# Performance work log

Hardware: AMD Instinct MI355X
Metric: run time of the kernel (lower is better)

Reference implementation:

```python
import jax, jax.numpy as jnp
import numpy as np

B, Q, K, H = 4, 512, 512, 256

def setup_inputs() -> dict:
    key = jax.random.key(0)
    ks = jax.random.split(key, 6)
    scale = 1.0 / np.sqrt(H)
    return {
        "queries": jax.random.normal(ks[0], (B, Q, H), dtype=jnp.float32),
        "keys": jax.random.normal(ks[1], (B, K, H), dtype=jnp.float32),
        "values": jax.random.normal(ks[2], (B, K, H), dtype=jnp.float32),
        "W_q": jax.random.normal(ks[3], (H, H), dtype=jnp.float32) * scale,
        "W_k": jax.random.normal(ks[4], (H, H), dtype=jnp.float32) * scale,
        "w_v": jax.random.normal(ks[5], (H,), dtype=jnp.float32) * scale,
    }

def reference(queries, keys, values, W_q, W_k, w_v):
    # Linear (no bias): x @ W.T, matching torch nn.Linear convention
    q = jnp.einsum('bqh,oh->bqo', queries, W_q)      # [B,Q,H]
    k = jnp.einsum('bkh,oh->bko', keys, W_k)          # [B,K,H]
    # broadcast add -> tanh -> linear reduce to scores [B,Q,K]
    features = jnp.tanh(q[:, :, None, :] + k[:, None, :, :])  # [B,Q,K,H]
    scores = jnp.einsum('bqkh,h->bqk', features, w_v)          # [B,Q,K]
    attn = jax.nn.softmax(scores, axis=-1)                     # [B,Q,K]
    # dropout p=0 (eval) -> identity
    return jnp.einsum('bqk,bkd->bqd', attn, values)            # [B,Q,Dv]
```

## Files before the change

### kernel.cpp

```cpp
#include <hip/hip_runtime.h>
#include <hip/hip_bf16.h>
#include <math.h>


#define B_ 4
#define Q_ 512
#define K_ 512
#define H_ 256
#define QE_ELEMS (B_ * Q_ * H_)
#define KE_ELEMS (B_ * H_ * K_)

static constexpr float CEXP = 2.8853900817779268f;
static constexpr float LOG2E = 1.4426950408889634f;

typedef float v2f __attribute__((ext_vector_type(2)));
typedef float v4f __attribute__((ext_vector_type(4)));

__device__ __forceinline__ v2f pk_fma(v2f a, v2f b, v2f c) {
    v2f d;
    asm("v_pk_fma_f32 %0, %1, %2, %3" : "=v"(d) : "v"(a), "v"(b), "v"(c));
    return d;
}
__device__ __forceinline__ v2f pk_fma_l(v2f a, v2f b, v2f c) {
    v2f d;
    asm("v_pk_fma_f32 %0, %1, %2, %3 op_sel:[0,0,0] op_sel_hi:[0,1,1]"
        : "=v"(d) : "v"(a), "v"(b), "v"(c));
    return d;
}
__device__ __forceinline__ v2f pk_fma_h(v2f a, v2f b, v2f c) {
    v2f d;
    asm("v_pk_fma_f32 %0, %1, %2, %3 op_sel:[1,0,0] op_sel_hi:[1,1,1]"
        : "=v"(d) : "v"(a), "v"(b), "v"(c));
    return d;
}
__device__ __forceinline__ v2f pk_mul(v2f a, v2f b) {
    v2f d;
    asm("v_pk_mul_f32 %0, %1, %2" : "=v"(d) : "v"(a), "v"(b));
    return d;
}
__device__ __forceinline__ v2f pk_mul_h(v2f a, v2f b) {
    v2f d;
    asm("v_pk_mul_f32 %0, %1, %2 op_sel:[1,0] op_sel_hi:[1,1]"
        : "=v"(d) : "v"(a), "v"(b));
    return d;
}

#define PJ_AS(team, buf, dd, row) smem[(((team)*2 + (buf)) * 16 + (dd)) * 68 + (row)]
#define PJ_SS(team, buf, dd, row) smem[8704 + (((team)*2 + (buf)) * 16 + (dd)) * 68 + (row)]

__global__ __launch_bounds__(1024, 4) void proj_exp(
    const float* __restrict__ queries, const float* __restrict__ keys,
    const float* __restrict__ Wq, const float* __restrict__ Wk,
    float* __restrict__ qe, float* __restrict__ ke)
{
    __shared__ __align__(16) float smem[17408];

    const int bid = blockIdx.x;
    const int team = threadIdx.x >> 8;
    const int tid = threadIdx.x & 255;

    const float* A; const float* S; float* C; int ldc;
    if (bid < 128) {
        int mt = bid >> 2, nt = bid & 3;
        A = queries + (mt * 64) * H_;
        S = Wq + (nt * 64) * H_;
        C = qe + (mt * 64) * H_ + nt * 64;
        ldc = H_;
    } else {
        int id = bid - 128;
        int b = id >> 5, mt = (id >> 3) & 3, nt = id & 7;
        A = Wk + (mt * 64) * H_;
        S = keys + ((long)(b * K_ + nt * 64)) * H_;
        C = ke + ((long)(b * H_ + mt * 64)) * K_ + nt * 64;
        ldc = K_;
    }

    const int tx = tid & 15;
    const int ty = tid >> 4;
    const int ldr = tid >> 2;
    const int ldd = (tid & 3) * 4;
    const float* GA = A + ldr * H_ + team * 64 + ldd;
    const float* GS = S + ldr * H_ + team * 64 + ldd;

    float4 av = *(const float4*)GA;
    float4 sv = *(const float4*)GS;
    PJ_AS(team, 0, ldd + 0, ldr) = av.x; PJ_AS(team, 0, ldd + 1, ldr) = av.y;
    PJ_AS(team, 0, ldd + 2, ldr) = av.z; PJ_AS(team, 0, ldd + 3, ldr) = av.w;
    PJ_SS(team, 0, ldd + 0, ldr) = sv.x; PJ_SS(team, 0, ldd + 1, ldr) = sv.y;
    PJ_SS(team, 0, ldd + 2, ldr) = sv.z; PJ_SS(team, 0, ldd + 3, ldr) = sv.w;

    float acc[4][4] = {};
#pragma unroll
    for (int c = 0; c < 4; ++c) {
        const int cur = c & 1;
        if (c < 3) {
            av = *(const float4*)(GA + (c + 1) * 16);
            sv = *(const float4*)(GS + (c + 1) * 16);
        }
        __syncthreads();
#pragma unroll
        for (int dd = 0; dd < 16; ++dd) {
            float4 a4 = *(const float4*)&PJ_AS(team, cur, dd, ty * 4);
            float4 b4 = *(const float4*)&PJ_SS(team, cur, dd, tx * 4);
            float am[4] = {a4.x, a4.y, a4.z, a4.w};
            float bn[4] = {b4.x, b4.y, b4.z, b4.w};
#pragma unroll
            for (int i = 0; i < 4; ++i)
#pragma unroll
                for (int j = 0; j < 4; ++j)
                    acc[i][j] = fmaf(am[i], bn[j], acc[i][j]);
        }
        if (c < 3) {
            const int nxt = cur ^ 1;
            PJ_AS(team, nxt, ldd + 0, ldr) = av.x;
            PJ_AS(team, nxt, ldd + 1, ldr) = av.y;
            PJ_AS(team, nxt, ldd + 2, ldr) = av.z;
            PJ_AS(team, nxt, ldd + 3, ldr) = av.w;
            PJ_SS(team, nxt, ldd + 0, ldr) = sv.x;
            PJ_SS(team, nxt, ldd + 1, ldr) = sv.y;
            PJ_SS(team, nxt, ldd + 2, ldr) = sv.z;
            PJ_SS(team, nxt, ldd + 3, ldr) = sv.w;
        }
    }

    __syncthreads();
    if (team > 0) {
        float* Cmb = smem + (team - 1) * 4352;
#pragma unroll
        for (int i = 0; i < 4; ++i) {
            float4 o = {acc[i][0], acc[i][1], acc[i][2], acc[i][3]};
            *(float4*)&Cmb[(ty * 4 + i) * 68 + tx * 4] = o;
        }
    }
    __syncthreads();
    if (team == 0) {
#pragma unroll
        for (int i = 0; i < 4; ++i) {
            const int off = (ty * 4 + i) * 68 + tx * 4;
            float4 p1 = *(const float4*)&smem[off];
            float4 p2 = *(const float4*)&smem[4352 + off];
            float4 p3 = *(const float4*)&smem[8704 + off];
            float4 o;
            o.x = __builtin_amdgcn_exp2f(CEXP * (acc[i][0] + p1.x + p2.x + p3.x));
            o.y = __builtin_amdgcn_exp2f(CEXP * (acc[i][1] + p1.y + p2.y + p3.y));
            o.z = __builtin_amdgcn_exp2f(CEXP * (acc[i][2] + p1.z + p2.z + p3.z));
            o.w = __builtin_amdgcn_exp2f(CEXP * (acc[i][3] + p1.w + p2.w + p3.w));
            *(float4*)&C[(ty * 4 + i) * ldc + tx * 4] = o;
        }
    }
}

__global__ __launch_bounds__(1024, 8) void attn(
    const float* __restrict__ qe, const float* __restrict__ ke,
    const float* __restrict__ values, const float* __restrict__ wv,
    float* __restrict__ out)
{
    const int bid = blockIdx.x;
    const int xcd = bid & 7;
    const int b = xcd >> 1;
    const int q0 = (((bid >> 3) << 1) | (xcd & 1)) * 4;
    const int t = threadIdx.x;

    __shared__ __align__(16) float smem[9472];
    float* sQ  = smem;
    float* wvs = smem + 4 * H_;
    float* sS  = smem + 5 * H_;
    float* sP  = smem + 5 * H_ + 4 * K_;

    sQ[t] = qe[((long)(b * Q_ + q0 + (t >> 8))) * H_ + (t & 255)];
    if (t < H_) wvs[t] = wv[t];
    __syncthreads();

    {
        const int k2 = (t & 255) * 2;
        const int g = t >> 8;
        const float* keb = ke + ((long)(b * H_ + g * 64)) * K_ + k2;

        v2f nx0 = *(const v2f*)(keb);
        v2f nx1 = *(const v2f*)(keb + K_);
        v2f nx2 = *(const v2f*)(keb + 2 * K_);
        v2f nx3 = *(const v2f*)(keb + 3 * K_);
        v2f acc[4] = {{0.f,0.f},{0.f,0.f},{0.f,0.f},{0.f,0.f}};
        const v2f one2 = {1.0f, 1.0f};

#pragma unroll 2
        for (int hl = 0; hl < 64; hl += 4) {
            v2f c0 = nx0, c1 = nx1, c2 = nx2, c3 = nx3;
            if (hl < 60) {
                const float* p = keb + (hl + 4) * K_;
                nx0 = *(const v2f*)(p);
                nx1 = *(const v2f*)(p + K_);
                nx2 = *(const v2f*)(p + 2 * K_);
                nx3 = *(const v2f*)(p + 3 * K_);
            }
            const int h = g * 64 + hl;
            v4f w4 = *(const v4f*)&wvs[h];
            const v2f wlo = w4.lo, whi = w4.hi;
#pragma unroll
            for (int q = 0; q < 4; ++q) {
                v4f e = *(const v4f*)&sQ[q * H_ + h];
                const v2f elo = e.lo, ehi = e.hi;
                v2f t0 = pk_fma_l(elo, c0, one2);
                v2f t1 = pk_fma_h(elo, c1, one2);
                v2f t2 = pk_fma_l(ehi, c2, one2);
                v2f t3 = pk_fma_h(ehi, c3, one2);
                v2f d01 = pk_mul(t0, t1);
                v2f d23 = pk_mul(t2, t3);
                v2f n01 = pk_fma_l(wlo, t1, pk_mul_h(wlo, t0));
                v2f n23 = pk_fma_l(whi, t3, pk_mul_h(whi, t2));
                v2f num = pk_fma(n01, d23, pk_mul(n23, d01));
                v2f den = pk_mul(d01, d23);
                v2f r;
                r.x = __builtin_amdgcn_rcpf(den.x);
                r.y = __builtin_amdgcn_rcpf(den.y);
                acc[q] = pk_fma(num, r, acc[q]);
            }
        }

        if (g > 0) {
            float* dst = sP + (g - 1) * 4 * K_;
#pragma unroll
            for (int q = 0; q < 4; ++q)
                *(v2f*)&dst[q * K_ + k2] = acc[q];
        }
        __syncthreads();
        if (g == 0) {
            const v2f m2 = {-2.0f, -2.0f};
#pragma unroll
            for (int q = 0; q < 4; ++q) {
                v2f p0 = *(const v2f*)&sP[0 * 4 * K_ + q * K_ + k2];
                v2f p1 = *(const v2f*)&sP[1 * 4 * K_ + q * K_ + k2];
                v2f p2 = *(const v2f*)&sP[2 * 4 * K_ + q * K_ + k2];
                v2f s = acc[q] + p0 + p1 + p2;
                *(v2f*)&sS[q * K_ + k2] = s * m2;
            }
        }
    }
    __syncthreads();

    if (t < 256) {
        const int lane = t & 63;
        const int q = t >> 6;
        float sv[8];
        float m = -INFINITY;
#pragma unroll
        for (int j = 0; j < 8; ++j) {
            sv[j] = sS[q * K_ + lane + 64 * j];
            m = fmaxf(m, sv[j]);
        }
#pragma unroll
        for (int off = 32; off >= 1; off >>= 1) m = fmaxf(m, __shfl_xor(m, off));
        float sum = 0.f;
#pragma unroll
        for (int j = 0; j < 8; ++j) {
            sv[j] = __builtin_amdgcn_exp2f((sv[j] - m) * LOG2E);
            sum += sv[j];
        }
#pragma unroll
        for (int off = 32; off >= 1; off >>= 1) sum += __shfl_xor(sum, off);
        float rs = 1.0f / sum;
#pragma unroll
        for (int j = 0; j < 8; ++j) sS[q * K_ + lane + 64 * j] = sv[j] * rs;
    }
    __syncthreads();

    {
        const int hp = t & 127;
        const int kq = t >> 7;
        const int kbeg = kq * 64;
        const float* vb = values + (long)b * K_ * H_ + hp * 2;

        v2f acc0 = {0.f, 0.f}, acc1 = {0.f, 0.f};
        v2f acc2 = {0.f, 0.f}, acc3 = {0.f, 0.f};
#pragma unroll 2
        for (int k = kbeg; k < kbeg + 64; k += 2) {
            v2f v0 = *(const v2f*)&vb[(k + 0) * H_];
            v2f v1 = *(const v2f*)&vb[(k + 1) * H_];
            v2f a0 = *(const v2f*)&sS[0 * K_ + k];
            v2f a1 = *(const v2f*)&sS[1 * K_ + k];
            v2f a2 = *(const v2f*)&sS[2 * K_ + k];
            v2f a3 = *(const v2f*)&sS[3 * K_ + k];
            acc0 = pk_fma_l(a0, v0, pk_fma_h(a0, v1, acc0));
            acc1 = pk_fma_l(a1, v0, pk_fma_h(a1, v1, acc1));
            acc2 = pk_fma_l(a2, v0, pk_fma_h(a2, v1, acc2));
            acc3 = pk_fma_l(a3, v0, pk_fma_h(a3, v1, acc3));
        }

        __syncthreads();
        float* sRed = smem;
        *(v2f*)&sRed[(kq * 4 + 0) * 256 + hp * 2] = acc0;
        *(v2f*)&sRed[(kq * 4 + 1) * 256 + hp * 2] = acc1;
        *(v2f*)&sRed[(kq * 4 + 2) * 256 + hp * 2] = acc2;
        *(v2f*)&sRed[(kq * 4 + 3) * 256 + hp * 2] = acc3;
        __syncthreads();

        const int q = t >> 8;
        const int h = t & 255;
        float s = 0.f;
#pragma unroll
        for (int kk = 0; kk < 8; ++kk)
            s += sRed[(kk * 4 + q) * 256 + h];
        out[((long)(b * Q_ + q0 + q)) * H_ + h] = s;
    }
}

extern "C" void kernel_launch(void* const* d_in, const int* in_sizes, int n_in,
                              void* d_out, int out_size, void* d_ws, size_t ws_size,
                              hipStream_t stream) {
    const float* queries = (const float*)d_in[0];
    const float* keys    = (const float*)d_in[1];
    const float* values  = (const float*)d_in[2];
    const float* Wq      = (const float*)d_in[3];
    const float* Wk      = (const float*)d_in[4];
    const float* wv      = (const float*)d_in[5];
    float* out = (float*)d_out;

    float* qe = (float*)d_ws;
    float* ke = qe + QE_ELEMS;

    proj_exp<<<256, 1024, 0, stream>>>(queries, keys, Wq, Wk, qe, ke);
    attn<<<512, 1024, 0, stream>>>(qe, ke, values, wv, out);
}
```

Before: 118.6 us.

## Fold score partial reduction into softmax and widen PV loop to float4 with prefetch

All four thread groups now write their score partials to shared memory, and the softmax threads sum them. This removes a barrier and the separate reduction pass by group 0. The attn·V stage switches from float2 to float4 value loads with 16 k-slices of 32, and prefetches value rows one iteration ahead. Shared memory grows from about 37 KB to 64 KB per block, which may limit occupancy. The final cross-slice reduction is doubled in length and uses split accumulators.

After: 113.1 us. 1.05x faster.

```diff
diff --git a/kernel.cpp b/kernel.cpp
--- a/kernel.cpp
+++ b/kernel.cpp
@@ -42,6 +42,18 @@
     v2f d;
     asm("v_pk_mul_f32 %0, %1, %2 op_sel:[1,0] op_sel_hi:[1,1]"
         : "=v"(d) : "v"(a), "v"(b));
+    return d;
+}
+__device__ __forceinline__ v4f pk4_fma_l(v2f a, v4f b, v4f c) {
+    v4f d;
+    d.lo = pk_fma_l(a, b.lo, c.lo);
+    d.hi = pk_fma_l(a, b.hi, c.hi);
+    return d;
+}
+__device__ __forceinline__ v4f pk4_fma_h(v2f a, v4f b, v4f c) {
+    v4f d;
+    d.lo = pk_fma_h(a, b.lo, c.lo);
+    d.hi = pk_fma_h(a, b.hi, c.hi);
     return d;
 }
 
@@ -161,7 +173,7 @@
     const int q0 = (((bid >> 3) << 1) | (xcd & 1)) * 4;
     const int t = threadIdx.x;
 
-    __shared__ __align__(16) float smem[9472];
+    __shared__ __align__(16) float smem[16384];
     float* sQ  = smem;
     float* wvs = smem + 4 * H_;
     float* sS  = smem + 5 * H_;
@@ -217,23 +229,11 @@
             }
         }
 
-        if (g > 0) {
-            float* dst = sP + (g - 1) * 4 * K_;
+        {
+            float* dst = sP + g * 4 * K_;
 #pragma unroll
             for (int q = 0; q < 4; ++q)
                 *(v2f*)&dst[q * K_ + k2] = acc[q];
-        }
-        __syncthreads();
-        if (g == 0) {
-            const v2f m2 = {-2.0f, -2.0f};
-#pragma unroll
-            for (int q = 0; q < 4; ++q) {
-                v2f p0 = *(const v2f*)&sP[0 * 4 * K_ + q * K_ + k2];
-                v2f p1 = *(const v2f*)&sP[1 * 4 * K_ + q * K_ + k2];
-                v2f p2 = *(const v2f*)&sP[2 * 4 * K_ + q * K_ + k2];
-                v2f s = acc[q] + p0 + p1 + p2;
-                *(v2f*)&sS[q * K_ + k2] = s * m2;
-            }
         }
     }
     __syncthreads();
@@ -245,7 +245,10 @@
         float m = -INFINITY;
 #pragma unroll
         for (int j = 0; j < 8; ++j) {
-            sv[j] = sS[q * K_ + lane + 64 * j];
+            const int idx = q * K_ + lane + 64 * j;
+            float p01 = sP[idx] + sP[4 * K_ + idx];
+            float p23 = sP[8 * K_ + idx] + sP[12 * K_ + idx];
+            sv[j] = -2.0f * (p01 + p23);
             m = fmaxf(m, sv[j]);
         }
 #pragma unroll
@@ -262,45 +265,69 @@
 #pragma unroll
         for (int j = 0; j < 8; ++j) sS[q * K_ + lane + 64 * j] = sv[j] * rs;
     }
+
+    const int h4 = (t & 63) * 4;
+    const int kq = t >> 6;
+    const int kbeg = kq * 32;
+    const float* vb = values + (long)b * K_ * H_ + h4;
+
+    v4f va = *(const v4f*)&vb[(kbeg + 0) * H_];
+    v4f vc = *(const v4f*)&vb[(kbeg + 1) * H_];
+
     __syncthreads();
 
     {
-        const int hp = t & 127;
-        const int kq = t >> 7;
-        const int kbeg = kq * 64;
-        const float* vb = values + (long)b * K_ * H_ + hp * 2;
-
-        v2f acc0 = {0.f, 0.f}, acc1 = {0.f, 0.f};
-        v2f acc2 = {0.f, 0.f}, acc3 = {0.f, 0.f};
-#pragma unroll 2
-        for (int k = kbeg; k < kbeg + 64; k += 2) {
-            v2f v0 = *(const v2f*)&vb[(k + 0) * H_];
-            v2f v1 = *(const v2f*)&vb[(k + 1) * H_];
-            v2f a0 = *(const v2f*)&sS[0 * K_ + k];
-            v2f a1 = *(const v2f*)&sS[1 * K_ + k];
-            v2f a2 = *(const v2f*)&sS[2 * K_ + k];
-            v2f a3 = *(const v2f*)&sS[3 * K_ + k];
-            acc0 = pk_fma_l(a0, v0, pk_fma_h(a0, v1, acc0));
-            acc1 = pk_fma_l(a1, v0, pk_fma_h(a1, v1, acc1));
-            acc2 = pk_fma_l(a2, v0, pk_fma_h(a2, v1, acc2));
-            acc3 = pk_fma_l(a3, v0, pk_fma_h(a3, v1, acc3));
+        v4f acc0 = {0.f,0.f,0.f,0.f}, acc1 = {0.f,0.f,0.f,0.f};
+        v4f acc2 = {0.f,0.f,0.f,0.f}, acc3 = {0.f,0.f,0.f,0.f};
+#pragma unroll 1
+        for (int k = kbeg; k < kbeg + 32; k += 4) {
+            v4f vd = *(const v4f*)&vb[(k + 2) * H_];
+            v4f ve = *(const v4f*)&vb[(k + 3) * H_];
+            {
+                v2f a0 = *(const v2f*)&sS[0 * K_ + k];
+                v2f a1 = *(const v2f*)&sS[1 * K_ + k];
+                v2f a2 = *(const v2f*)&sS[2 * K_ + k];
+                v2f a3 = *(const v2f*)&sS[3 * K_ + k];
+                acc0 = pk4_fma_l(a0, va, pk4_fma_h(a0, vc, acc0));
+                acc1 = pk4_fma_l(a1, va, pk4_fma_h(a1, vc, acc1));
+                acc2 = pk4_fma_l(a2, va, pk4_fma_h(a2, vc, acc2));
+                acc3 = pk4_fma_l(a3, va, pk4_fma_h(a3, vc, acc3));
+            }
+            if (k + 4 < kbeg + 32) {
+                va = *(const v4f*)&vb[(k + 4) * H_];
+                vc = *(const v4f*)&vb[(k + 5) * H_];
+            }
+            {
+                v2f a0 = *(const v2f*)&sS[0 * K_ + k + 2];
+                v2f a1 = *(const v2f*)&sS[1 * K_ + k + 2];
+                v2f a2 = *(const v2f*)&sS[2 * K_ + k + 2];
+                v2f a3 = *(const v2f*)&sS[3 * K_ + k + 2];
+                acc0 = pk4_fma_l(a0, vd, pk4_fma_h(a0, ve, acc0));
+                acc1 = pk4_fma_l(a1, vd, pk4_fma_h(a1, ve, acc1));
+                acc2 = pk4_fma_l(a2, vd, pk4_fma_h(a2, ve, acc2));
+                acc3 = pk4_fma_l(a3, vd, pk4_fma_h(a3, ve, acc3));
+            }
         }
 
         __syncthreads();
         float* sRed = smem;
-        *(v2f*)&sRed[(kq * 4 + 0) * 256 + hp * 2] = acc0;
-        *(v2f*)&sRed[(kq * 4 + 1) * 256 + hp * 2] = acc1;
-        *(v2f*)&sRed[(kq * 4 + 2) * 256 + hp * 2] = acc2;
-        *(v2f*)&sRed[(kq * 4 + 3) * 256 + hp * 2] = acc3;
+        *(v4f*)&sRed[(kq * 4 + 0) * 256 + h4] = acc0;
+        *(v4f*)&sRed[(kq * 4 + 1) * 256 + h4] = acc1;
+        *(v4f*)&sRed[(kq * 4 + 2) * 256 + h4] = acc2;
+        *(v4f*)&sRed[(kq * 4 + 3) * 256 + h4] = acc3;
         __syncthreads();
 
         const int q = t >> 8;
         const int h = t & 255;
-        float s = 0.f;
-#pragma unroll
-        for (int kk = 0; kk < 8; ++kk)
-            s += sRed[(kk * 4 + q) * 256 + h];
-        out[((long)(b * Q_ + q0 + q)) * H_ + h] = s;
+        float s0 = 0.f, s1 = 0.f, s2 = 0.f, s3 = 0.f;
+#pragma unroll
+        for (int kk = 0; kk < 16; kk += 4) {
+            s0 += sRed[((kk + 0) * 4 + q) * 256 + h];
+            s1 += sRed[((kk + 1) * 4 + q) * 256 + h];
+            s2 += sRed[((kk + 2) * 4 + q) * 256 + h];
+            s3 += sRed[((kk + 3) * 4 + q) * 256 + h];
+        }
+        out[((long)(b * Q_ + q0 + q)) * H_ + h] = (s0 + s1) + (s2 + s3);
     }
 }
 
```
